# Kernel optimization log

Hardware: AMD Instinct MI355X
Metric: run time of the kernel (lower is better)

Reference implementation:

```python
import jax, jax.numpy as jnp
import numpy as np

D_MODEL = 1024
N_HEADS = 16
FEA = 512
BATCH = 16
D_FF = 2048
HALF = D_MODEL // 2  # d_model / 2**fd_num with fd_num=1
INV_SQRT2 = 1.0 / np.sqrt(2.0).astype(np.float32)


def conv1d_circ(x, w, b):
    # x: (B, C_in, L); w: (C_out, C_in, 3); circular padding of 1 each side
    xp = jnp.pad(x, ((0, 0), (0, 0), (1, 1)), mode='wrap')
    y = jax.lax.conv_general_dilated(xp, w, (1,), 'VALID',
                                     dimension_numbers=('NCH', 'OIH', 'NCH'))
    return y + b[None, :, None]


def layer_norm(x, g, b):
    m = jnp.mean(x, axis=-1, keepdims=True)
    v = jnp.mean((x - m) ** 2, axis=-1, keepdims=True)
    return (x - m) / jnp.sqrt(v + 1e-5) * g + b


def setup_inputs() -> dict:
    key = jax.random.key(0)
    ks = jax.random.split(key, 16)
    s = 0.02
    inp = {
        'x': jax.random.normal(ks[0], (BATCH, FEA, D_MODEL), dtype=jnp.float32),
        'Wq': jax.random.normal(ks[1], (D_MODEL, HALF, 3), dtype=jnp.float32) * s,
        'bq': jnp.zeros((D_MODEL,), jnp.float32),
        'Wk': jax.random.normal(ks[2], (D_MODEL, HALF, 3), dtype=jnp.float32) * s,
        'bk': jnp.zeros((D_MODEL,), jnp.float32),
        'Wv': jax.random.normal(ks[3], (D_MODEL, HALF, 3), dtype=jnp.float32) * s,
        'bv': jnp.zeros((D_MODEL,), jnp.float32),
        'uns_w': jax.random.normal(ks[4], (FEA, 2 * FEA, 3), dtype=jnp.float32) * s,
        'uns_b': jnp.zeros((FEA,), jnp.float32),
        'cv_w1': jax.random.normal(ks[5], (D_FF, D_MODEL, 3), dtype=jnp.float32) * s,
        'cv_b1': jnp.zeros((D_FF,), jnp.float32),
        'cv_w2': jax.random.normal(ks[6], (HALF, D_FF, 3), dtype=jnp.float32) * s,
        'cv_b2': jnp.zeros((HALF,), jnp.float32),
        'cv_g': jnp.ones((HALF,), jnp.float32),
        'cv_beta': jnp.zeros((HALF,), jnp.float32),
        'up_w1': jax.random.normal(ks[7], (D_FF, HALF, 3), dtype=jnp.float32) * s,
        'up_b1': jnp.zeros((D_FF,), jnp.float32),
        'up_w2': jax.random.normal(ks[8], (D_MODEL, D_FF, 3), dtype=jnp.float32) * s,
        'up_b2': jnp.zeros((D_MODEL,), jnp.float32),
        'up_g': jnp.ones((D_MODEL,), jnp.float32),
        'up_beta': jnp.zeros((D_MODEL,), jnp.float32),
    }
    return inp


def reference(x, Wq, bq, Wk, bk, Wv, bv, uns_w, uns_b,
              cv_w1, cv_b1, cv_w2, cv_b2, cv_g, cv_beta,
              up_w1, up_b1, up_w2, up_b2, up_g, up_beta):
    x_input = x
    # torch code detaches x before the wavelet transform -> no grad through this branch
    xd = jax.lax.stop_gradient(x)
    # Haar (db1) single-level DWT along last axis (even length -> exact pairwise)
    x1 = (xd[..., 0::2] + xd[..., 1::2]) * INV_SQRT2  # cA: (B, F, HALF)
    x2 = (xd[..., 0::2] - xd[..., 1::2]) * INV_SQRT2  # cD: (B, F, HALF)

    def proj(z, w, b):  # (B, F, HALF) -> (B, F, D_MODEL)
        return conv1d_circ(z.swapaxes(1, 2), w, b).swapaxes(1, 2)

    def heads(z):  # (B, F, D_MODEL) -> (B, H, F, dh)
        b_, f_, _ = z.shape
        return z.reshape(b_, f_, N_HEADS, -1).transpose(0, 2, 1, 3)

    qh, kh, vh = heads(proj(x1, Wq, bq)), heads(proj(x1, Wk, bk)), heads(proj(x1, Wv, bv))
    ql, kl, vl = heads(proj(x2, Wq, bq)), heads(proj(x2, Wk, bk)), heads(proj(x2, Wv, bv))

    scale = 1.0 / np.sqrt(N_HEADS).astype(np.float32)  # note: module scales by sqrt(n_heads)
    b_, f_ = x.shape[0], x.shape[1]

    hp = jax.nn.softmax(jnp.einsum('bhqd,bhkd->bhqk', qh, kl) * scale, axis=-1)
    h_ctx = jnp.einsum('bhqk,bhkd->bhqd', hp, vh).transpose(0, 2, 1, 3).reshape(b_, f_, -1)
    lp = jax.nn.softmax(jnp.einsum('bhqd,bhkd->bhqk', ql, kh) * scale, axis=-1)
    l_ctx = jnp.einsum('bhqk,bhkd->bhqd', lp, vl).transpose(0, 2, 1, 3).reshape(b_, f_, -1)

    ctx = jnp.concatenate([h_ctx, l_ctx], axis=1)          # (B, 2F, D_MODEL)
    ctx = conv1d_circ(ctx, uns_w, uns_b)                    # channels=2F -> F, length=D_MODEL

    # Convlayer: conv over fea axis, channels D_MODEL -> D_FF -> HALF, then LN
    h = conv1d_circ(ctx.swapaxes(1, 2), cv_w1, cv_b1)
    h = conv1d_circ(jax.nn.relu(h), cv_w2, cv_b2)
    ctx = layer_norm(h.swapaxes(1, 2), cv_g, cv_beta)       # (B, F, HALF)

    # upsizeConvlayer: HALF -> D_FF -> D_MODEL, then LN
    h = conv1d_circ(ctx.swapaxes(1, 2), up_w1, up_b1)
    h = conv1d_circ(jax.nn.relu(h), up_w2, up_b2)
    out = layer_norm(h.swapaxes(1, 2), up_g, up_beta)       # (B, F, D_MODEL)
    return out + x_input
```

## Files before the change

### kernel.cpp

```cpp
#include <hip/hip_runtime.h>
#include <hip/hip_bf16.h>

#define B_    16
#define FEA_  512
#define DM_   1024
#define HALF_ 512
#define DFF_  2048

typedef unsigned short u16;
typedef __attribute__((ext_vector_type(8))) short bf16x8;
typedef __attribute__((ext_vector_type(4))) float f32x4;

__device__ __forceinline__ float bf2f(u16 u) {
  union { unsigned int i; float f; } v; v.i = ((unsigned int)u) << 16; return v.f;
}
__device__ __forceinline__ u16 f2bf(float f) {
  union { float f; unsigned int i; } v; v.f = f;
  unsigned int x = v.i;
  return (u16)((x + 0x7fffu + ((x >> 16) & 1u)) >> 16);
}
__device__ __forceinline__ void gload16(const u16* g, u16* l) {
  __builtin_amdgcn_global_load_lds(
      (const __attribute__((address_space(1))) void*)g,
      (__attribute__((address_space(3))) void*)l, 16, 0, 0);
}

__global__ void dwt_kernel(const float* __restrict__ x, u16* __restrict__ x1,
                           u16* __restrict__ x2, int n) {
  int i = blockIdx.x * 256 + threadIdx.x;
  if (i >= n) return;
  float2 v = ((const float2*)x)[i];
  x1[i] = f2bf((v.x + v.y) * 0.70710678118f);
  x2[i] = f2bf((v.x - v.y) * 0.70710678118f);
}

__global__ void wtrans3_kernel(const float* __restrict__ w0, const float* __restrict__ w1,
                               const float* __restrict__ w2, u16* __restrict__ wt,
                               int Cout, int Cin) {
  int n = Cout * Cin * 3;
  int e = blockIdx.x * 256 + threadIdx.x;
  if (e >= 3 * n) return;
  int i = e / n, le = e - i * n;
  const float* w = (i == 0) ? w0 : ((i == 1) ? w1 : w2);
  int co = le / (Cin * 3);
  int r  = le - co * Cin * 3;
  int ci = r / 3;
  int t  = r - ci * 3;
  wt[(size_t)i * n + ((size_t)t * Cout + co) * Cin + ci] = f2bf(w[le]);
}

struct WTSeg { const float* src; u16* dst; int cout, cin, base; };
struct WT5 { WTSeg s[5]; int total; };
__global__ void wtrans5_kernel(WT5 p) {
  int e = blockIdx.x * 256 + threadIdx.x;
  if (e >= p.total) return;
#pragma unroll
  for (int i = 0; i < 5; ++i) {
    int Cin = p.s[i].cin, Cout = p.s[i].cout;
    int n = Cout * Cin * 3;
    int le = e - p.s[i].base;
    if (le >= 0 && le < n) {
      int co = le / (Cin * 3);
      int r  = le - co * Cin * 3;
      int ci = r / 3;
      int t  = r - ci * 3;
      p.s[i].dst[((size_t)t * Cout + co) * Cin + ci] = f2bf(p.s[i].src[le]);
    }
  }
}

#define ZS_GLOAD(c0_)                                                        \
  {                                                                          \
    _Pragma("unroll") for (int i_ = 0; i_ < 5; ++i_) {                       \
      int e_ = tid + i_ * 256;                                               \
      if (e_ < 130 * 8) {                                                    \
        int r_ = e_ >> 3, c_ = e_ & 7;                                       \
        int gl_ = l0 + r_ - 1;                                               \
        if (gl_ < 0) gl_ += L; else if (gl_ >= L) gl_ -= L;                  \
        gload16(Zb + (size_t)gl_ * Cin + (c0_) + ((c_ ^ (r_ & 7)) * 8),      \
                smem + ((size_t)(i_ * 256 + (tid & 192)) * 8));              \
      }                                                                      \
    }                                                                        \
  }
#define WS_ISSUE(t_, c0_, buf_)                                              \
  {                                                                          \
    const u16* Wg_ = Wt + ((size_t)(t_) * Cout + co0) * Cin + (c0_);         \
    int c_ = lane & 7;                                                       \
    _Pragma("unroll") for (int i_ = 0; i_ < 4; ++i_) {                       \
      int rw_ = (i_ * 4 + w) * 8 + (lane >> 3);                              \
      gload16(Wg_ + (size_t)rw_ * Cin + ((c_ ^ (rw_ & 7)) * 8),              \
              &Wb[(buf_)][(i_ * 4 + w) * 8][0]);                             \
    }                                                                        \
  }

__global__ __launch_bounds__(256, 2) void conv_mfma_kernel(
    const u16* __restrict__ Z, const u16* __restrict__ Wt,
    const float* __restrict__ bias, u16* __restrict__ out,
    int L, int Cin, int Cout, int osl, int osc, int relu) {
  __shared__ __align__(16) u16 smem[130 * 64 + 3 * 128 * 64];
  u16 (*Zs)[64] = (u16(*)[64])smem;
  u16 (*Wb)[128][64] = (u16(*)[128][64])(smem + 130 * 64);
  int l0 = blockIdx.x * 128, co0 = blockIdx.y * 128, b = blockIdx.z;
  int tid = threadIdx.x;
  int lane = tid & 63, w = tid >> 6, wr = w >> 1, wc = w & 1;
  int row16 = lane & 15, g4 = lane >> 4;
  f32x4 acc[4][4];
#pragma unroll
  for (int i = 0; i < 4; ++i)
#pragma unroll
    for (int j = 0; j < 4; ++j) acc[i][j] = (f32x4){0.f, 0.f, 0.f, 0.f};
  const u16* Zb = Z + (size_t)b * L * Cin;

  int nchunk = (Cin >> 6) * 3;
  ZS_GLOAD(0);
  WS_ISSUE(0, 0, 0);
  WS_ISSUE(1, 0, 1);

  for (int k = 0; k < nchunk; ++k) {
    int t = k % 3;
    int c0 = (k / 3) << 6;
    int cur = k % 3;
    if (k + 1 < nchunk) asm volatile("s_waitcnt vmcnt(4)" ::: "memory");
    else                asm volatile("s_waitcnt vmcnt(0)" ::: "memory");
    __builtin_amdgcn_s_barrier();
#pragma unroll
    for (int ks = 0; ks < 2; ++ks) {
      int s = ks * 4 + g4;
      bf16x8 af[4], bfr[4];
#pragma unroll
      for (int mi = 0; mi < 4; ++mi) {
        int ra = wr * 64 + mi * 16 + row16 + t;
        af[mi] = *(const bf16x8*)&Zs[ra][(s ^ (ra & 7)) * 8];
      }
#pragma unroll
      for (int ni = 0; ni < 4; ++ni) {
        int rb = wc * 64 + ni * 16 + row16;
        bfr[ni] = *(const bf16x8*)&Wb[cur][rb][(s ^ (rb & 7)) * 8];
      }
      __builtin_amdgcn_s_setprio(1);
#pragma unroll
      for (int mi = 0; mi < 4; ++mi)
#pragma unroll
        for (int ni = 0; ni < 4; ++ni)
          acc[mi][ni] = __builtin_amdgcn_mfma_f32_16x16x32_bf16(
              af[mi], bfr[ni], acc[mi][ni], 0, 0, 0);
      __builtin_amdgcn_s_setprio(0);
    }
    if ((t == 2) && (c0 + 64 < Cin)) {
      __builtin_amdgcn_s_barrier();
      ZS_GLOAD(c0 + 64);
    }
    if (k + 2 < nchunk) WS_ISSUE((k + 2) % 3, ((k + 2) / 3) << 6, (k + 2) % 3);
  }

  __syncthreads();
  const int TP = 136;
  u16* tile = smem;
  size_t ob = (size_t)b * L * Cout;
  int S, rowbase, colbase;
  if (osc == 1) { S = osl; rowbase = l0; colbase = co0; }
  else          { S = osc; rowbase = co0; colbase = l0; }
#pragma unroll
  for (int ni = 0; ni < 4; ++ni) {
    int c_loc = wc * 64 + ni * 16 + row16;
    float bz = bias[co0 + c_loc];
#pragma unroll
    for (int mi = 0; mi < 4; ++mi) {
#pragma unroll
      for (int r = 0; r < 4; ++r) {
        int l_loc = wr * 64 + mi * 16 + g4 * 4 + r;
        float v = acc[mi][ni][r] + bz;
        if (relu) v = fmaxf(v, 0.f);
        int row = (osc == 1) ? l_loc : c_loc;
        int col = (osc == 1) ? c_loc : l_loc;
        tile[row * TP + col] = f2bf(v);
      }
    }
  }
  __syncthreads();
  for (int e = tid; e < 128 * 16; e += 256) {
    int row = e >> 4, c8 = (e & 15) * 8;
    *(uint4*)(out + ob + (size_t)(rowbase + row) * S + colbase + c8) =
        *(const uint4*)&tile[row * TP + c8];
  }
}

__global__ __launch_bounds__(256, 4) void attn_mfma_kernel(
    const u16* __restrict__ qh, const u16* __restrict__ kh, const u16* __restrict__ vhT,
    const u16* __restrict__ ql, const u16* __restrict__ kl, const u16* __restrict__ vlT,
    u16* __restrict__ ctx) {
  __shared__ u16 Qs[64][72], Ks[64][72], Vts[64][72];
  __shared__ u16 Ps[64][72];
  __shared__ float rsl[2][2][32];
  int qt = blockIdx.x, h = blockIdx.y, bz = blockIdx.z;
  int b = bz >> 1, br = bz & 1;
  const u16* Q  = br ? ql  : qh;
  const u16* K  = br ? kh  : kl;
  const u16* Vt = br ? vlT : vhT;
  int tid = threadIdx.x;
  int lane = tid & 63, w = tid >> 6, wr = w >> 1, wc = w & 1;
  int row16 = lane & 15, g4 = lane >> 4, k8 = g4 * 8;
  int q0 = qt * 64;
  size_t baseQK = (size_t)b * FEA_ * DM_ + h * 64;
  size_t baseV  = (size_t)b * DM_ * FEA_ + (size_t)(h * 64) * FEA_;
  for (int e = tid; e < 64 * 8; e += 256) {
    int r = e >> 3, c = e & 7;
    *(uint4*)&Qs[r][c * 8] = *(const uint4*)(Q + baseQK + (size_t)(q0 + r) * DM_ + c * 8);
  }
  f32x4 oacc[2][2];
  float rsum[2][4];
#pragma unroll
  for (int i = 0; i < 2; ++i) {
#pragma unroll
    for (int j = 0; j < 2; ++j) oacc[i][j] = (f32x4){0.f, 0.f, 0.f, 0.f};
#pragma unroll
    for (int r = 0; r < 4; ++r) rsum[i][r] = 0.f;
  }
  for (int kt = 0; kt < 8; ++kt) {
    __syncthreads();
    for (int e = tid; e < 64 * 8; e += 256) {
      int r = e >> 3, c = e & 7;
      *(uint4*)&Ks[r][c * 8]  = *(const uint4*)(K + baseQK + (size_t)(kt * 64 + r) * DM_ + c * 8);
      *(uint4*)&Vts[r][c * 8] = *(const uint4*)(Vt + baseV + (size_t)r * FEA_ + kt * 64 + c * 8);
    }
    __syncthreads();
    f32x4 sacc[2][2];
#pragma unroll
    for (int i = 0; i < 2; ++i)
#pragma unroll
      for (int j = 0; j < 2; ++j) sacc[i][j] = (f32x4){0.f, 0.f, 0.f, 0.f};
#pragma unroll
    for (int ks = 0; ks < 2; ++ks) {
      int k0 = ks * 32 + k8;
      bf16x8 a0 = *(const bf16x8*)&Qs[wr * 32 + row16][k0];
      bf16x8 a1 = *(const bf16x8*)&Qs[wr * 32 + 16 + row16][k0];
      bf16x8 b0 = *(const bf16x8*)&Ks[wc * 32 + row16][k0];
      bf16x8 b1 = *(const bf16x8*)&Ks[wc * 32 + 16 + row16][k0];
      sacc[0][0] = __builtin_amdgcn_mfma_f32_16x16x32_bf16(a0, b0, sacc[0][0], 0, 0, 0);
      sacc[0][1] = __builtin_amdgcn_mfma_f32_16x16x32_bf16(a0, b1, sacc[0][1], 0, 0, 0);
      sacc[1][0] = __builtin_amdgcn_mfma_f32_16x16x32_bf16(a1, b0, sacc[1][0], 0, 0, 0);
      sacc[1][1] = __builtin_amdgcn_mfma_f32_16x16x32_bf16(a1, b1, sacc[1][1], 0, 0, 0);
    }
#pragma unroll
    for (int mi = 0; mi < 2; ++mi)
#pragma unroll
      for (int ni = 0; ni < 2; ++ni)
#pragma unroll
        for (int r = 0; r < 4; ++r) {
          float p = __expf(sacc[mi][ni][r] * 0.25f);
          rsum[mi][r] += p;
          Ps[wr * 32 + mi * 16 + g4 * 4 + r][wc * 32 + ni * 16 + row16] = f2bf(p);
        }
    __syncthreads();
#pragma unroll
    for (int ks = 0; ks < 2; ++ks) {
      int k0 = ks * 32 + k8;
      bf16x8 a0 = *(const bf16x8*)&Ps[wr * 32 + row16][k0];
      bf16x8 a1 = *(const bf16x8*)&Ps[wr * 32 + 16 + row16][k0];
      bf16x8 b0 = *(const bf16x8*)&Vts[wc * 32 + row16][k0];
      bf16x8 b1 = *(const bf16x8*)&Vts[wc * 32 + 16 + row16][k0];
      oacc[0][0] = __builtin_amdgcn_mfma_f32_16x16x32_bf16(a0, b0, oacc[0][0], 0, 0, 0);
      oacc[0][1] = __builtin_amdgcn_mfma_f32_16x16x32_bf16(a0, b1, oacc[0][1], 0, 0, 0);
      oacc[1][0] = __builtin_amdgcn_mfma_f32_16x16x32_bf16(a1, b0, oacc[1][0], 0, 0, 0);
      oacc[1][1] = __builtin_amdgcn_mfma_f32_16x16x32_bf16(a1, b1, oacc[1][1], 0, 0, 0);
    }
  }
#pragma unroll
  for (int mi = 0; mi < 2; ++mi)
#pragma unroll
    for (int r = 0; r < 4; ++r) {
#pragma unroll
      for (int m = 1; m < 16; m <<= 1) rsum[mi][r] += __shfl_xor(rsum[mi][r], m);
    }
  if (row16 == 0) {
#pragma unroll
    for (int mi = 0; mi < 2; ++mi)
#pragma unroll
      for (int r = 0; r < 4; ++r) rsl[wr][wc][mi * 16 + g4 * 4 + r] = rsum[mi][r];
  }
  __syncthreads();
#pragma unroll
  for (int mi = 0; mi < 2; ++mi)
#pragma unroll
    for (int ni = 0; ni < 2; ++ni)
#pragma unroll
      for (int r = 0; r < 4; ++r) {
        int qq = mi * 16 + g4 * 4 + r;
        float denom = rsl[wr][0][qq] + rsl[wr][1][qq];
        float o = oacc[mi][ni][r] / denom;
        Ps[wc * 32 + ni * 16 + row16][wr * 32 + qq] = f2bf(o);
      }
  __syncthreads();
  for (int e = tid; e < 64 * 8; e += 256) {
    int r = e >> 3, c = e & 7;
    size_t dst = ((size_t)b * DM_ + h * 64 + r) * (2 * FEA_) + br * 512 + q0 + c * 8;
    *(uint4*)(ctx + dst) = *(const uint4*)&Ps[r][c * 8];
  }
}

template <int RESID>
__global__ void ln_kernel(const u16* __restrict__ in, const float* __restrict__ g,
                          const float* __restrict__ beta, const float* __restrict__ resid,
                          void* __restrict__ outp, int C) {
  int row = blockIdx.x;
  int tid = threadIdx.x;
  const u16* p = in + (size_t)row * C;
  float s = 0.f, ss = 0.f;
  for (int c = tid; c < C; c += 256) {
    float v = bf2f(p[c]);
    s += v; ss += v * v;
  }
#pragma unroll
  for (int m = 1; m < 64; m <<= 1) { s += __shfl_xor(s, m); ss += __shfl_xor(ss, m); }
  __shared__ float red[2][4];
  int wid = tid >> 6, lane = tid & 63;
  if (lane == 0) { red[0][wid] = s; red[1][wid] = ss; }
  __syncthreads();
  s  = red[0][0] + red[0][1] + red[0][2] + red[0][3];
  ss = red[1][0] + red[1][1] + red[1][2] + red[1][3];
  float m  = s / C;
  float var = ss / C - m * m;
  float inv = rsqrtf(var + 1e-5f);
  for (int c = tid; c < C; c += 256) {
    float v = (bf2f(p[c]) - m) * inv * g[c] + beta[c];
    if (RESID) ((float*)outp)[(size_t)row * C + c] = v + resid[(size_t)row * C + c];
    else       ((u16*)outp)[(size_t)row * C + c]   = f2bf(v);
  }
}

extern "C" void kernel_launch(void* const* d_in, const int* in_sizes, int n_in,
                              void* d_out, int out_size, void* d_ws, size_t ws_size,
                              hipStream_t stream) {
  (void)in_sizes; (void)n_in; (void)out_size; (void)ws_size;
  const float* x      = (const float*)d_in[0];
  const float* Wq     = (const float*)d_in[1];
  const float* bq     = (const float*)d_in[2];
  const float* Wk     = (const float*)d_in[3];
  const float* bk     = (const float*)d_in[4];
  const float* Wv     = (const float*)d_in[5];
  const float* bv     = (const float*)d_in[6];
  const float* uns_w  = (const float*)d_in[7];
  const float* uns_b  = (const float*)d_in[8];
  const float* cv_w1  = (const float*)d_in[9];
  const float* cv_b1  = (const float*)d_in[10];
  const float* cv_w2  = (const float*)d_in[11];
  const float* cv_b2  = (const float*)d_in[12];
  const float* cv_g   = (const float*)d_in[13];
  const float* cv_beta= (const float*)d_in[14];
  const float* up_w1  = (const float*)d_in[15];
  const float* up_b1  = (const float*)d_in[16];
  const float* up_w2  = (const float*)d_in[17];
  const float* up_b2  = (const float*)d_in[18];
  const float* up_g   = (const float*)d_in[19];
  const float* up_beta= (const float*)d_in[20];

  char* ws = (char*)d_ws;
  const size_t MB = 1ull << 20;
  u16* x1    = (u16*)(ws + 0);
  u16* x1x2  = x1;
  u16* qhb   = (u16*)(ws + 16 * MB);
  u16* khb   = (u16*)(ws + 48 * MB);
  u16* vhb   = (u16*)(ws + 80 * MB);
  u16* qlb   = (u16*)(ws + 32 * MB);
  u16* klb   = (u16*)(ws + 64 * MB);
  u16* vlb   = (u16*)(ws + 96 * MB);
  u16* wt_proj = (u16*)d_out;
  u16* ctx   = (u16*)d_out;
  u16* wt_uns  = (u16*)(ws + 0);
  u16* wt_cv1  = (u16*)(ws + 4 * MB);
  u16* wt_cv2  = (u16*)(ws + 17 * MB);
  u16* wt_up1  = (u16*)(ws + 24 * MB);
  u16* wt_up2  = (u16*)(ws + 31 * MB);
  u16* ctx2  = (u16*)(ws + 48 * MB);
  u16* h1    = (u16*)(ws + 64 * MB);
  u16* h2    = (u16*)(ws + 96 * MB);
  u16* ctx3  = (u16*)(ws + 104 * MB);
  u16* h3    = (u16*)(ws + 64 * MB);
  u16* h4    = (u16*)(ws + 48 * MB);

  dwt_kernel<<<(B_ * FEA_ * HALF_ + 255) / 256, 256, 0, stream>>>(x, x1, (u16*)(ws + 8 * MB),
                                                                  B_ * FEA_ * HALF_);

  const int NPROJ = DM_ * HALF_ * 3;
  wtrans3_kernel<<<(3 * NPROJ + 255) / 256, 256, 0, stream>>>(Wq, Wk, Wv, wt_proj, DM_, HALF_);

  auto conv = [&](const u16* Z, const u16* wt, const float* bias, u16* out, int L,
                  int Cin, int Cout, int osl, int osc, int relu, int nb) {
    conv_mfma_kernel<<<dim3(L / 128, Cout / 128, nb), 256, 0, stream>>>(
        Z, wt, bias, out, L, Cin, Cout, osl, osc, relu);
  };

  conv(x1x2, wt_proj,              bq, qhb, FEA_, HALF_, DM_, DM_, 1, 0, 32);
  conv(x1x2, wt_proj + NPROJ,      bk, khb, FEA_, HALF_, DM_, DM_, 1, 0, 32);
  conv(x1x2, wt_proj + 2 * NPROJ,  bv, vhb, FEA_, HALF_, DM_, 1, FEA_, 0, 32);

  attn_mfma_kernel<<<dim3(8, 16, 32), 256, 0, stream>>>(qhb, khb, vhb, qlb, klb, vlb, ctx);

  WT5 p;
  int base = 0;
  auto seg = [&](int i, const float* src, u16* dst, int cout, int cin) {
    p.s[i] = {src, dst, cout, cin, base};
    base += cout * cin * 3;
  };
  seg(0, uns_w, wt_uns, FEA_, 2 * FEA_);
  seg(1, cv_w1, wt_cv1, DFF_, DM_);
  seg(2, cv_w2, wt_cv2, HALF_, DFF_);
  seg(3, up_w1, wt_up1, DFF_, HALF_);
  seg(4, up_w2, wt_up2, DM_, DFF_);
  p.total = base;
  wtrans5_kernel<<<(p.total + 255) / 256, 256, 0, stream>>>(p);

  conv(ctx, wt_uns, uns_b, ctx2, DM_, 2 * FEA_, FEA_, 1, DM_, 0, B_);

  conv(ctx2, wt_cv1, cv_b1, h1, FEA_, DM_, DFF_, DFF_, 1, 1, B_);
  conv(h1, wt_cv2, cv_b2, h2, FEA_, DFF_, HALF_, HALF_, 1, 0, B_);
  ln_kernel<0><<<B_ * FEA_, 256, 0, stream>>>(h2, cv_g, cv_beta, nullptr, ctx3, HALF_);

  conv(ctx3, wt_up1, up_b1, h3, FEA_, HALF_, DFF_, DFF_, 1, 1, B_);
  conv(h3, wt_up2, up_b2, h4, FEA_, DFF_, DM_, DM_, 1, 0, B_);
  ln_kernel<1><<<B_ * FEA_, 256, 0, stream>>>(h4, up_g, up_beta, x, d_out, DM_);
}
```

Baseline: 713.0 us.

## Unroll conv K-loop by tap with register-held A fragments, vectorize layernorm

Restructures the conv MFMA main loop so each 64-channel group is processed as three explicit tap stages. The third tap's activation fragments are preloaded into registers, which lets the next activation tile load start before the final compute and removes a separate barrier round. The layernorm kernel also switches to 4-wide vector loads and stores. The price is extra register pressure from holding eight A fragments, and more intricate wait/barrier ordering that could introduce races if the counts are wrong.

```diff
diff --git a/kernel.cpp b/kernel.cpp
--- a/kernel.cpp
+++ b/kernel.cpp
@@ -92,6 +92,46 @@
               &Wb[(buf_)][(i_ * 4 + w) * 8][0]);                             \
     }                                                                        \
   }
+#define COMPUTE(t_, buf_)                                                    \
+  {                                                                          \
+    _Pragma("unroll") for (int ks = 0; ks < 2; ++ks) {                       \
+      int s = ks * 4 + g4;                                                   \
+      bf16x8 af[4], bfr[4];                                                  \
+      _Pragma("unroll") for (int mi = 0; mi < 4; ++mi) {                     \
+        int ra = wr * 64 + mi * 16 + row16 + (t_);                           \
+        af[mi] = *(const bf16x8*)&Zs[ra][(s ^ (ra & 7)) * 8];                \
+      }                                                                      \
+      _Pragma("unroll") for (int ni = 0; ni < 4; ++ni) {                     \
+        int rb = wc * 64 + ni * 16 + row16;                                  \
+        bfr[ni] = *(const bf16x8*)&Wb[(buf_)][rb][(s ^ (rb & 7)) * 8];       \
+      }                                                                      \
+      __builtin_amdgcn_s_setprio(1);                                         \
+      _Pragma("unroll") for (int mi = 0; mi < 4; ++mi)                       \
+        _Pragma("unroll") for (int ni = 0; ni < 4; ++ni)                     \
+          acc[mi][ni] = __builtin_amdgcn_mfma_f32_16x16x32_bf16(             \
+              af[mi], bfr[ni], acc[mi][ni], 0, 0, 0);                        \
+      __builtin_amdgcn_s_setprio(0);                                         \
+    }                                                                        \
+  }
+#define COMPUTE2_REG(buf_)                                                   \
+  {                                                                          \
+    _Pragma("unroll") for (int ks = 0; ks < 2; ++ks) {                       \
+      int s = ks * 4 + g4;                                                   \
+      bf16x8 bfr[4];                                                         \
+      _Pragma("unroll") for (int ni = 0; ni < 4; ++ni) {                     \
+        int rb = wc * 64 + ni * 16 + row16;                                  \
+        bfr[ni] = *(const bf16x8*)&Wb[(buf_)][rb][(s ^ (rb & 7)) * 8];       \
+      }                                                                      \
+      __builtin_amdgcn_s_setprio(1);                                         \
+      _Pragma("unroll") for (int mi = 0; mi < 4; ++mi)                       \
+        _Pragma("unroll") for (int ni = 0; ni < 4; ++ni)                     \
+          acc[mi][ni] = __builtin_amdgcn_mfma_f32_16x16x32_bf16(             \
+              af2[ks * 4 + mi], bfr[ni], acc[mi][ni], 0, 0, 0);              \
+      __builtin_amdgcn_s_setprio(0);                                         \
+    }                                                                        \
+  }
+#define WAIT4 { asm volatile("s_waitcnt vmcnt(4)" ::: "memory");             \
+                __builtin_amdgcn_s_barrier(); }
 
 __global__ __launch_bounds__(256, 2) void conv_mfma_kernel(
     const u16* __restrict__ Z, const u16* __restrict__ Wt,
@@ -111,46 +151,43 @@
     for (int j = 0; j < 4; ++j) acc[i][j] = (f32x4){0.f, 0.f, 0.f, 0.f};
   const u16* Zb = Z + (size_t)b * L * Cin;
 
-  int nchunk = (Cin >> 6) * 3;
+  int ncg = Cin >> 6;
   ZS_GLOAD(0);
   WS_ISSUE(0, 0, 0);
   WS_ISSUE(1, 0, 1);
 
-  for (int k = 0; k < nchunk; ++k) {
-    int t = k % 3;
-    int c0 = (k / 3) << 6;
-    int cur = k % 3;
-    if (k + 1 < nchunk) asm volatile("s_waitcnt vmcnt(4)" ::: "memory");
-    else                asm volatile("s_waitcnt vmcnt(0)" ::: "memory");
-    __builtin_amdgcn_s_barrier();
-#pragma unroll
-    for (int ks = 0; ks < 2; ++ks) {
-      int s = ks * 4 + g4;
-      bf16x8 af[4], bfr[4];
-#pragma unroll
-      for (int mi = 0; mi < 4; ++mi) {
-        int ra = wr * 64 + mi * 16 + row16 + t;
-        af[mi] = *(const bf16x8*)&Zs[ra][(s ^ (ra & 7)) * 8];
+  for (int cg = 0; cg < ncg; ++cg) {
+    int c0 = cg << 6;
+    bool lastg = (cg == ncg - 1);
+    WAIT4;
+    WS_ISSUE(2, c0, 2);
+    COMPUTE(0, 0);
+    WAIT4;
+    if (!lastg) WS_ISSUE(0, c0 + 64, 0);
+    COMPUTE(1, 1);
+    if (!lastg) {
+      WAIT4;
+      bf16x8 af2[8];
+#pragma unroll
+      for (int ks = 0; ks < 2; ++ks) {
+        int s = ks * 4 + g4;
+#pragma unroll
+        for (int mi = 0; mi < 4; ++mi) {
+          int ra = wr * 64 + mi * 16 + row16 + 2;
+          af2[ks * 4 + mi] = *(const bf16x8*)&Zs[ra][(s ^ (ra & 7)) * 8];
+        }
       }
-#pragma unroll
-      for (int ni = 0; ni < 4; ++ni) {
-        int rb = wc * 64 + ni * 16 + row16;
-        bfr[ni] = *(const bf16x8*)&Wb[cur][rb][(s ^ (rb & 7)) * 8];
-      }
-      __builtin_amdgcn_s_setprio(1);
-#pragma unroll
-      for (int mi = 0; mi < 4; ++mi)
-#pragma unroll
-        for (int ni = 0; ni < 4; ++ni)
-          acc[mi][ni] = __builtin_amdgcn_mfma_f32_16x16x32_bf16(
-              af[mi], bfr[ni], acc[mi][ni], 0, 0, 0);
-      __builtin_amdgcn_s_setprio(0);
-    }
-    if ((t == 2) && (c0 + 64 < Cin)) {
+      __builtin_amdgcn_sched_barrier(0);
+      asm volatile("s_waitcnt lgkmcnt(0)" ::: "memory");
       __builtin_amdgcn_s_barrier();
       ZS_GLOAD(c0 + 64);
-    }
-    if (k + 2 < nchunk) WS_ISSUE((k + 2) % 3, ((k + 2) / 3) << 6, (k + 2) % 3);
+      WS_ISSUE(1, c0 + 64, 1);
+      COMPUTE2_REG(2);
+    } else {
+      asm volatile("s_waitcnt vmcnt(0)" ::: "memory");
+      __builtin_amdgcn_s_barrier();
+      COMPUTE(2, 2);
+    }
   }
 
   __syncthreads();
@@ -306,9 +343,11 @@
   int tid = threadIdx.x;
   const u16* p = in + (size_t)row * C;
   float s = 0.f, ss = 0.f;
-  for (int c = tid; c < C; c += 256) {
-    float v = bf2f(p[c]);
-    s += v; ss += v * v;
+  for (int c = tid * 4; c < C; c += 1024) {
+    ushort4 u = *(const ushort4*)(p + c);
+    float v0 = bf2f(u.x), v1 = bf2f(u.y), v2 = bf2f(u.z), v3 = bf2f(u.w);
+    s += v0 + v1 + v2 + v3;
+    ss += v0 * v0 + v1 * v1 + v2 * v2 + v3 * v3;
   }
 #pragma unroll
   for (int m = 1; m < 64; m <<= 1) { s += __shfl_xor(s, m); ss += __shfl_xor(ss, m); }
@@ -321,10 +360,22 @@
   float m  = s / C;
   float var = ss / C - m * m;
   float inv = rsqrtf(var + 1e-5f);
-  for (int c = tid; c < C; c += 256) {
-    float v = (bf2f(p[c]) - m) * inv * g[c] + beta[c];
-    if (RESID) ((float*)outp)[(size_t)row * C + c] = v + resid[(size_t)row * C + c];
-    else       ((u16*)outp)[(size_t)row * C + c]   = f2bf(v);
+  for (int c = tid * 4; c < C; c += 1024) {
+    ushort4 u = *(const ushort4*)(p + c);
+    float4 gg = *(const float4*)(g + c);
+    float4 bb = *(const float4*)(beta + c);
+    float v0 = (bf2f(u.x) - m) * inv * gg.x + bb.x;
+    float v1 = (bf2f(u.y) - m) * inv * gg.y + bb.y;
+    float v2 = (bf2f(u.z) - m) * inv * gg.z + bb.z;
+    float v3 = (bf2f(u.w) - m) * inv * gg.w + bb.w;
+    if (RESID) {
+      float4 rr = *(const float4*)(resid + (size_t)row * C + c);
+      float4 o = {v0 + rr.x, v1 + rr.y, v2 + rr.z, v3 + rr.w};
+      *(float4*)((float*)outp + (size_t)row * C + c) = o;
+    } else {
+      ushort4 o = {f2bf(v0), f2bf(v1), f2bf(v2), f2bf(v3)};
+      *(ushort4*)((u16*)outp + (size_t)row * C + c) = o;
+    }
   }
 }
 
```

Result: faster. 663.6 us (-6.9%).
